# Optimization experiments

Hardware: AMD Instinct MI355X
Metric: run time of the kernel (lower is better)

Reference implementation:

```python
import jax, jax.numpy as jnp
import numpy as np

B, N, W, D, H, E = 8, 10000, 12, 16, 128, 160000
OUT = D  # out_dim must equal in_dim per the reshape in forward


def setup_inputs() -> dict:
    key = jax.random.key(0)
    ks = jax.random.split(key, 13)
    s_ih = 1.0 / np.sqrt(H)
    return {
        "x": jax.random.normal(ks[0], (B, N, W, D), jnp.float32),
        "edge_index": jax.random.randint(ks[1], (2, E), 0, N, dtype=jnp.int64),
        "edge_weight": jax.random.uniform(ks[2], (E,), jnp.float32),
        "W_ih": jax.random.uniform(ks[3], (4 * H, D), jnp.float32, -s_ih, s_ih),
        "W_hh": jax.random.uniform(ks[4], (4 * H, H), jnp.float32, -s_ih, s_ih),
        "b_ih": jax.random.uniform(ks[5], (4 * H,), jnp.float32, -s_ih, s_ih),
        "b_hh": jax.random.uniform(ks[6], (4 * H,), jnp.float32, -s_ih, s_ih),
        "gcn1_w": jax.random.normal(ks[7], (H, H), jnp.float32) * s_ih,
        "gcn1_b": jnp.zeros((H,), jnp.float32),
        "gcn2_w": jax.random.normal(ks[8], (H, H), jnp.float32) * s_ih,
        "gcn2_b": jnp.zeros((H,), jnp.float32),
        "fc_w": jax.random.uniform(ks[9], (OUT, H), jnp.float32, -s_ih, s_ih),
        "fc_b": jax.random.uniform(ks[10], (OUT,), jnp.float32, -s_ih, s_ih),
    }


def reference(x, edge_index, edge_weight, W_ih, W_hh, b_ih, b_hh,
              gcn1_w, gcn1_b, gcn2_w, gcn2_b, fc_w, fc_b):
    Bb, Nn, T, Din = x.shape
    Hh = W_hh.shape[1]
    xs = x.reshape(Bb * Nn, T, Din)

    # --- LSTM over time, keep final hidden state (torch gate order i,f,g,o) ---
    bias = b_ih + b_hh
    def step(carry, xt):
        h, c = carry
        z = xt @ W_ih.T + h @ W_hh.T + bias  # (B*N, 4H)
        i, f, g, o = jnp.split(z, 4, axis=-1)
        c = jax.nn.sigmoid(f) * c + jax.nn.sigmoid(i) * jnp.tanh(g)
        h = jax.nn.sigmoid(o) * jnp.tanh(c)
        return (h, c), None
    h0 = jnp.zeros((Bb * Nn, Hh), x.dtype)
    (h_last, _), _ = jax.lax.scan(step, (h0, h0), jnp.swapaxes(xs, 0, 1))
    h = h_last.reshape(Bb, Nn, Hh)

    # --- GCN normalization with added self-loops (PyG GCNConv semantics) ---
    src, dst = edge_index[0], edge_index[1]
    loop = jnp.arange(Nn)
    src_f = jnp.concatenate([src, loop])
    dst_f = jnp.concatenate([dst, loop])
    w_f = jnp.concatenate([edge_weight, jnp.ones((Nn,), edge_weight.dtype)])
    deg = jnp.zeros((Nn,), w_f.dtype).at[dst_f].add(w_f)
    dinv = jnp.where(deg > 0, jax.lax.rsqrt(jnp.where(deg > 0, deg, 1.0)), 0.0)
    norm = dinv[src_f] * w_f * dinv[dst_f]  # (E+N,)

    def gcn(hx, wgt, b):
        xl = hx @ wgt.T                                  # (B, N, H)
        msg = xl[:, src_f, :] * norm[None, :, None]      # (B, E+N, H)
        agg = jnp.zeros_like(xl).at[:, dst_f, :].add(msg)
        return agg + b

    h = jax.nn.relu(gcn(h, gcn1_w, gcn1_b))
    h = jax.nn.relu(gcn(h, gcn2_w, gcn2_b))
    out = h @ fc_w.T + fc_b                              # (B, N, out_dim)
    return out
```

## Files before the change

### kernel.cpp

```cpp
#include <hip/hip_runtime.h>
#include <math.h>

#define NB 8
#define NN 10000
#define NT 12
#define ND 16
#define NH 128
#define NE 160000
#define BN (NB * NN)

typedef __attribute__((ext_vector_type(8))) short short8v;
typedef __attribute__((ext_vector_type(4))) float f32x4;
typedef unsigned short u16;

#define NL2E  -1.442695041f
#define N2L2E -2.885390082f

__device__ __forceinline__ u16 bf16_rn(float f) {
    unsigned int u = __float_as_uint(f);
    u += 0x7fffu + ((u >> 16) & 1u);
    return (u16)(u >> 16);
}
__device__ __forceinline__ float bf16f(u16 s) {
    return __uint_as_float((unsigned int)s << 16);
}
__device__ __forceinline__ unsigned int pack_split(float f) {
    unsigned int u = __float_as_uint(f);
    unsigned int hh = u >> 16;
    float rem = f - __uint_as_float(u & 0xffff0000u);
    unsigned int hl = bf16_rn(rem);
    return (hl << 16) | hh;
}

__global__ void prep_w_k(const float* __restrict__ Whh, const float* __restrict__ Wih,
                         const float* __restrict__ g1w, const float* __restrict__ g2w,
                         u16* __restrict__ whh_hi, u16* __restrict__ wih_hi2,
                         u16* __restrict__ g1hi, u16* __restrict__ g2hi,
                         float* __restrict__ deg, int* __restrict__ cnt, int* __restrict__ fill)
{
    int i = blockIdx.x * 256 + threadIdx.x;
    if (i < 512 * 128) {
        int j = i >> 7;
        float s = ((j >> 7) == 2) ? N2L2E : NL2E;
        whh_hi[i] = bf16_rn(s * Whh[i]);
    }
    if (i < 512 * 16) {
        int row = i >> 4, d = i & 15;
        float s = ((row >> 7) == 2) ? N2L2E : NL2E;
        u16 h = bf16_rn(s * Wih[i]);
        wih_hi2[row * 32 + d] = h;
        wih_hi2[row * 32 + 16 + d] = h;
    }
    if (i < 128 * 128) {
        g1hi[i] = bf16_rn(g1w[i]);
        g2hi[i] = bf16_rn(g2w[i]);
    }
    if (i < NN) { deg[i] = 1.0f; cnt[i] = 0; fill[i] = 0; }
}

__global__ __launch_bounds__(512, 2) void lstm4d_k(
    const float* __restrict__ x,
    const u16* __restrict__ whh_hi, const u16* __restrict__ wih_hi2,
    const float* __restrict__ bih, const float* __restrict__ bhh,
    u16* __restrict__ hhi_g)
{
    __shared__ __align__(16) u16 Hhi[2][64][128];
    __shared__ __align__(16) u16 Hx[2][64][40];
    const int tid = threadIdx.x;
    const int lane = tid & 63;
    const int wid = tid >> 6;
    const int j0 = wid * 16;
    const int l15 = lane & 15;
    const int lg = lane >> 4;
    const long seq0 = (long)blockIdx.x * 64;
    const int swzr = (l15 & 7) << 3;
    const int xs_seq = tid >> 3;
    const int xd0 = (tid & 7) * 2;

    short8v Bh[4][4];
    short8v b1[4];
    float bv[4];
#pragma unroll
    for (int kt = 0; kt < 4; ++kt)
#pragma unroll
        for (int g = 0; g < 4; ++g) {
            int row = g * NH + j0 + l15;
            Bh[kt][g] = *(const short8v*)(whh_hi + row * NH + kt * 32 + 8 * lg);
        }
#pragma unroll
    for (int g = 0; g < 4; ++g) {
        int row = g * NH + j0 + l15;
        b1[g] = *(const short8v*)(wih_hi2 + row * 32 + 8 * lg);
        bv[g] = (bih[row] + bhh[row]) * ((g == 2) ? N2L2E : NL2E);
    }

    {
        float2 xv = *(const float2*)(x + ((seq0 + xs_seq) * NT + 0) * ND + xd0);
        unsigned int p0 = pack_split(xv.x), p1 = pack_split(xv.y);
        *(ushort2*)&Hx[0][xs_seq][xd0] = make_ushort2((u16)p0, (u16)p1);
        *(ushort2*)&Hx[0][xs_seq][16 + xd0] = make_ushort2((u16)(p0 >> 16), (u16)(p1 >> 16));
    }
    f32x4 c[4];
#pragma unroll
    for (int m = 0; m < 4; ++m) c[m] = (f32x4){0.f, 0.f, 0.f, 0.f};
    __syncthreads();

    for (int t = 0; t < NT; ++t) {
        const int cur = t & 1, nxt = cur ^ 1;
        float2 xv;
        if (t + 1 < NT)
            xv = *(const float2*)(x + ((seq0 + xs_seq) * NT + (t + 1)) * ND + xd0);

#pragma unroll
        for (int m = 0; m < 4; ++m) {
            const int sq = m * 16 + l15;
            short8v xa = *(const short8v*)&Hx[cur][sq][8 * lg];

            f32x4 acc[4];
#pragma unroll
            for (int g = 0; g < 4; ++g)
                acc[g] = (f32x4){bv[g], bv[g], bv[g], bv[g]};

            if (t > 0) {
#pragma unroll
                for (int kt = 0; kt < 4; ++kt) {
                    const int kk = (kt * 32 + 8 * lg) ^ swzr;
                    short8v ah = *(const short8v*)&Hhi[cur][sq][kk];
#pragma unroll
                    for (int g = 0; g < 4; ++g)
                        acc[g] = __builtin_amdgcn_mfma_f32_16x16x32_bf16(ah, Bh[kt][g], acc[g], 0, 0, 0);
                }
            }
#pragma unroll
            for (int g = 0; g < 4; ++g)
                acc[g] = __builtin_amdgcn_mfma_f32_16x16x32_bf16(xa, b1[g], acc[g], 0, 0, 0);

#pragma unroll
            for (int r = 0; r < 4; ++r) {
                const float ui = exp2f(acc[0][r]);
                const float uf = exp2f(acc[1][r]);
                const float ug = exp2f(acc[2][r]);
                const float uo = exp2f(acc[3][r]);
                const float di = 1.f + ui, df = 1.f + uf;
                const float dg = 1.f + ug, dd = 1.f + uo;
                const float r0 = __builtin_amdgcn_rcpf(di * df);
                const float r1 = __builtin_amdgcn_rcpf(dg * dd);
                const float si = r0 * df;
                const float sf = r0 * di;
                const float tg = fmaf(2.f, r1 * dd, -1.f);
                const float so = r1 * dg;
                const float cc = fmaf(sf, c[m][r], si * tg);
                c[m][r] = cc;
                const float uc = exp2f(cc * N2L2E);
                const float rc = __builtin_amdgcn_rcpf(1.f + uc);
                const float hv = fmaf(2.f, so * rc, -so);
                const int sq2 = m * 16 + 4 * lg + r;
                const int jj = (j0 + l15) ^ ((sq2 & 7) << 3);
                Hhi[nxt][sq2][jj] = bf16_rn(hv);
            }
        }

        if (t + 1 < NT) {
            unsigned int p0 = pack_split(xv.x), p1 = pack_split(xv.y);
            *(ushort2*)&Hx[nxt][xs_seq][xd0] = make_ushort2((u16)p0, (u16)p1);
            *(ushort2*)&Hx[nxt][xs_seq][16 + xd0] = make_ushort2((u16)(p0 >> 16), (u16)(p1 >> 16));
        }
        __syncthreads();
    }

    for (int ci = tid; ci < 1024; ci += 512) {
        int s = ci >> 4, g16 = ci & 15;
        int sg = g16 ^ (s & 7);
        unsigned int sglob = (unsigned int)(seq0 + s);
        unsigned int b = sglob / NN;
        unsigned int n = sglob - b * NN;
        uint4 v = *(const uint4*)&Hhi[0][s][sg * 8];
        *(uint4*)(hhi_g + ((long)n * 8 + b) * NH + g16 * 8) = v;
    }
}

__global__ __launch_bounds__(512) void gemmx4_k(
    const u16* __restrict__ Ah, const u16* __restrict__ Whi,
    u16* __restrict__ out)
{
    const int tid = threadIdx.x;
    const int lane = tid & 63;
    const int wid = tid >> 6;
    const int j0 = wid * 16;
    const int l15 = lane & 15;
    const int lg = lane >> 4;
    const long row0 = (long)blockIdx.x * 64;

    short8v Bh[4];
#pragma unroll
    for (int kt = 0; kt < 4; ++kt)
        Bh[kt] = *(const short8v*)(Whi + (j0 + l15) * NH + kt * 32 + 8 * lg);

#pragma unroll
    for (int m = 0; m < 4; ++m) {
        f32x4 acc = (f32x4){0.f, 0.f, 0.f, 0.f};
#pragma unroll
        for (int kt = 0; kt < 4; ++kt) {
            long ar = (row0 + m * 16 + l15) * NH + kt * 32 + 8 * lg;
            short8v ah = *(const short8v*)(Ah + ar);
            acc = __builtin_amdgcn_mfma_f32_16x16x32_bf16(ah, Bh[kt], acc, 0, 0, 0);
        }
#pragma unroll
        for (int r = 0; r < 4; ++r)
            out[(row0 + m * 16 + 4 * lg + r) * NH + j0 + l15] = bf16_rn(acc[r]);
    }
}

__global__ void degacc_k(const int* __restrict__ ei, const float* __restrict__ ew,
                         float* deg, int* cnt) {
    int e = blockIdx.x * 256 + threadIdx.x;
    if (e < NE) {
        int d = ei[NE + e];
        atomicAdd(&deg[d], ew[e]);
        atomicAdd(&cnt[d], 1);
    }
}

__global__ __launch_bounds__(1024) void scan_k(const int* __restrict__ cnt,
                                               int* __restrict__ rowp,
                                               const float* __restrict__ deg,
                                               float* __restrict__ dinv) {
    for (int idx = threadIdx.x; idx < NN; idx += 1024) {
        float d = deg[idx];
        dinv[idx] = d > 0.f ? rsqrtf(d) : 0.f;
    }
    __shared__ int sA[1024];
    __shared__ int sB[1024];
    const int tid = threadIdx.x;
    const int CH = 10;
    int base = tid * CH;
    int local[CH];
    int ssum = 0;
#pragma unroll
    for (int i = 0; i < CH; ++i) {
        int idx = base + i;
        int v = (idx < NN) ? cnt[idx] : 0;
        local[i] = v; ssum += v;
    }
    int* src = sA; int* dst = sB;
    src[tid] = ssum;
    __syncthreads();
    for (int off = 1; off < 1024; off <<= 1) {
        int v = src[tid];
        if (tid >= off) v += src[tid - off];
        dst[tid] = v;
        __syncthreads();
        int* tmp = src; src = dst; dst = tmp;
    }
    int run = src[tid] - ssum;
#pragma unroll
    for (int i = 0; i < CH; ++i) {
        int idx = base + i;
        if (idx < NN) rowp[idx] = run;
        run += local[i];
    }
    if (tid == 1023) rowp[NN] = src[1023];
}

__global__ void scatter_k(const int* __restrict__ ei, const float* __restrict__ ew,
                          const float* __restrict__ dinv, const int* __restrict__ rowp,
                          int* fill, int* __restrict__ col, float* __restrict__ val)
{
    int e = blockIdx.x * 256 + threadIdx.x;
    if (e >= NE) return;
    int srcn = ei[e], d = ei[NE + e];
    int pos = rowp[d] + atomicAdd(&fill[d], 1);
    col[pos] = srcn;
    val[pos] = dinv[srcn] * ew[e] * dinv[d];
}

template<int EMIT>
__global__ __launch_bounds__(256) void gather6_k(const u16* __restrict__ xlb,
    const int* __restrict__ rowp, const int* __restrict__ col,
    const float* __restrict__ val, const float* __restrict__ dinv,
    const float* __restrict__ bias,
    u16* __restrict__ ohi,
    const float* __restrict__ fcw, const float* __restrict__ fcb,
    float* __restrict__ out)
{
    __shared__ float hrow[8][132];
    __shared__ float wl[16][132];
    const int n = blockIdx.x;
    const int tid = threadIdx.x;
    const int q = tid & 31;
    if (EMIT == 1) {
        for (int l = tid; l < 16 * 128; l += 256)
            wl[l >> 7][l & 127] = fcw[l];
    }
    const float dn = dinv[n];
    const float sn = dn * dn;
    float4 acc;
    {
        ushort4 u = *(const ushort4*)(xlb + (long)n * 1024 + tid * 4);
        acc.x = sn * bf16f(u.x); acc.y = sn * bf16f(u.y);
        acc.z = sn * bf16f(u.z); acc.w = sn * bf16f(u.w);
    }
    int e = rowp[n];
    const int e1 = rowp[n + 1];
    for (; e + 2 <= e1; e += 2) {
        const int s0 = col[e], s1 = col[e + 1];
        const float w0 = val[e], w1 = val[e + 1];
        const ushort4 u0 = *(const ushort4*)(xlb + (long)s0 * 1024 + tid * 4);
        const ushort4 u1 = *(const ushort4*)(xlb + (long)s1 * 1024 + tid * 4);
        acc.x = fmaf(w0, bf16f(u0.x), acc.x); acc.y = fmaf(w0, bf16f(u0.y), acc.y);
        acc.z = fmaf(w0, bf16f(u0.z), acc.z); acc.w = fmaf(w0, bf16f(u0.w), acc.w);
        acc.x = fmaf(w1, bf16f(u1.x), acc.x); acc.y = fmaf(w1, bf16f(u1.y), acc.y);
        acc.z = fmaf(w1, bf16f(u1.z), acc.z); acc.w = fmaf(w1, bf16f(u1.w), acc.w);
    }
    if (e < e1) {
        const int s0 = col[e];
        const float w0 = val[e];
        const ushort4 u0 = *(const ushort4*)(xlb + (long)s0 * 1024 + tid * 4);
        acc.x = fmaf(w0, bf16f(u0.x), acc.x); acc.y = fmaf(w0, bf16f(u0.y), acc.y);
        acc.z = fmaf(w0, bf16f(u0.z), acc.z); acc.w = fmaf(w0, bf16f(u0.w), acc.w);
    }
    const float4 bb = ((const float4*)bias)[q];
    const float o0 = fmaxf(acc.x + bb.x, 0.f);
    const float o1 = fmaxf(acc.y + bb.y, 0.f);
    const float o2 = fmaxf(acc.z + bb.z, 0.f);
    const float o3 = fmaxf(acc.w + bb.w, 0.f);
    if (EMIT == 0) {
        ushort4 h4 = make_ushort4(bf16_rn(o0), bf16_rn(o1), bf16_rn(o2), bf16_rn(o3));
        *(ushort4*)(ohi + (long)n * 1024 + tid * 4) = h4;
    } else {
        const int b = tid >> 5;
        *(float4*)&hrow[b][q * 4] = make_float4(o0, o1, o2, o3);
        __syncthreads();
        if (tid < 128) {
            const int b2 = tid >> 4, o = tid & 15;
            float a = fcb[o];
#pragma unroll 8
            for (int k = 0; k < NH; ++k) a = fmaf(hrow[b2][k], wl[o][k], a);
            out[((long)b2 * NN + n) * 16 + o] = a;
        }
    }
}

extern "C" void kernel_launch(void* const* d_in, const int* in_sizes, int n_in,
                              void* d_out, int out_size, void* d_ws, size_t ws_size,
                              hipStream_t stream)
{
    const float* x   = (const float*)d_in[0];
    const int*   ei  = (const int*)d_in[1];
    const float* ew  = (const float*)d_in[2];
    const float* Wih = (const float*)d_in[3];
    const float* Whh = (const float*)d_in[4];
    const float* bih = (const float*)d_in[5];
    const float* bhh = (const float*)d_in[6];
    const float* g1w = (const float*)d_in[7];
    const float* g1b = (const float*)d_in[8];
    const float* g2w = (const float*)d_in[9];
    const float* g2b = (const float*)d_in[10];
    const float* fcw = (const float*)d_in[11];
    const float* fcb = (const float*)d_in[12];
    float* out = (float*)d_out;

    char* ws = (char*)d_ws;
    u16* whh_hi  = (u16*)(ws + 0);
    u16* wih_hi2 = (u16*)(ws + 131072);
    u16* g1hi    = (u16*)(ws + 196608);
    u16* g2hi    = (u16*)(ws + 229376);
    float* deg   = (float*)(ws + 262144);
    float* dinv  = (float*)(ws + 303104);
    int*   cnt   = (int*)(ws + 344064);
    int*   fill  = (int*)(ws + 385024);
    int*   rowp  = (int*)(ws + 425984);
    int*   col   = (int*)(ws + 466176);
    float* val   = (float*)(ws + 1106176);
    u16* hhi     = (u16*)(ws + 2097152);
    u16* xlb     = (u16*)(ws + 22577152);

    prep_w_k<<<256, 256, 0, stream>>>(Whh, Wih, g1w, g2w, whh_hi, wih_hi2,
                                      g1hi, g2hi, deg, cnt, fill);
    lstm4d_k<<<BN / 64, 512, 0, stream>>>(x, whh_hi, wih_hi2, bih, bhh, hhi);

    degacc_k<<<(NE + 255) / 256, 256, 0, stream>>>(ei, ew, deg, cnt);
    scan_k<<<1, 1024, 0, stream>>>(cnt, rowp, deg, dinv);
    scatter_k<<<(NE + 255) / 256, 256, 0, stream>>>(ei, ew, dinv, rowp, fill, col, val);

    gemmx4_k<<<BN / 64, 512, 0, stream>>>(hhi, g1hi, xlb);
    gather6_k<0><<<NN, 256, 0, stream>>>(xlb, rowp, col, val, dinv, g1b,
                                         hhi, nullptr, nullptr, nullptr);
    gemmx4_k<<<BN / 64, 512, 0, stream>>>(hhi, g2hi, xlb);
    gather6_k<1><<<NN, 256, 0, stream>>>(xlb, rowp, col, val, dinv, g2b,
                                         nullptr, fcw, fcb, out);
}
```

Baseline: 477.3 us.

## Fuse GCN weight GEMM into gather kernel by aggregating before transform

```diff
diff --git a/kernel.cpp b/kernel.cpp
--- a/kernel.cpp
+++ b/kernel.cpp
@@ -179,38 +179,6 @@
     }
 }
 
-__global__ __launch_bounds__(512) void gemmx4_k(
-    const u16* __restrict__ Ah, const u16* __restrict__ Whi,
-    u16* __restrict__ out)
-{
-    const int tid = threadIdx.x;
-    const int lane = tid & 63;
-    const int wid = tid >> 6;
-    const int j0 = wid * 16;
-    const int l15 = lane & 15;
-    const int lg = lane >> 4;
-    const long row0 = (long)blockIdx.x * 64;
-
-    short8v Bh[4];
-#pragma unroll
-    for (int kt = 0; kt < 4; ++kt)
-        Bh[kt] = *(const short8v*)(Whi + (j0 + l15) * NH + kt * 32 + 8 * lg);
-
-#pragma unroll
-    for (int m = 0; m < 4; ++m) {
-        f32x4 acc = (f32x4){0.f, 0.f, 0.f, 0.f};
-#pragma unroll
-        for (int kt = 0; kt < 4; ++kt) {
-            long ar = (row0 + m * 16 + l15) * NH + kt * 32 + 8 * lg;
-            short8v ah = *(const short8v*)(Ah + ar);
-            acc = __builtin_amdgcn_mfma_f32_16x16x32_bf16(ah, Bh[kt], acc, 0, 0, 0);
-        }
-#pragma unroll
-        for (int r = 0; r < 4; ++r)
-            out[(row0 + m * 16 + 4 * lg + r) * NH + j0 + l15] = bf16_rn(acc[r]);
-    }
-}
-
 __global__ void degacc_k(const int* __restrict__ ei, const float* __restrict__ ew,
                          float* deg, int* cnt) {
     int e = blockIdx.x * 256 + threadIdx.x;
@@ -274,63 +242,93 @@
     val[pos] = dinv[srcn] * ew[e] * dinv[d];
 }
 
-template<int EMIT>
-__global__ __launch_bounds__(256) void gather6_k(const u16* __restrict__ xlb,
+template<int LAST>
+__global__ __launch_bounds__(256) void gcn_fused_k(const u16* __restrict__ hin,
     const int* __restrict__ rowp, const int* __restrict__ col,
     const float* __restrict__ val, const float* __restrict__ dinv,
-    const float* __restrict__ bias,
-    u16* __restrict__ ohi,
+    const float* __restrict__ bias, const u16* __restrict__ Whi,
+    u16* __restrict__ hout,
     const float* __restrict__ fcw, const float* __restrict__ fcb,
     float* __restrict__ out)
 {
+    __shared__ __align__(16) u16 Ag[16][128];
+    __shared__ __align__(16) u16 Ou[8][128];
     __shared__ float hrow[8][132];
     __shared__ float wl[16][132];
     const int n = blockIdx.x;
     const int tid = threadIdx.x;
+    const int b = tid >> 5;
     const int q = tid & 31;
-    if (EMIT == 1) {
+
+    if (tid < 128) *(uint4*)&Ag[8 + (tid >> 4)][(tid & 15) * 8] = make_uint4(0, 0, 0, 0);
+    if (LAST) {
         for (int l = tid; l < 16 * 128; l += 256)
             wl[l >> 7][l & 127] = fcw[l];
     }
+
     const float dn = dinv[n];
     const float sn = dn * dn;
-    float4 acc;
+    float4 accA, accB = make_float4(0.f, 0.f, 0.f, 0.f);
     {
-        ushort4 u = *(const ushort4*)(xlb + (long)n * 1024 + tid * 4);
-        acc.x = sn * bf16f(u.x); acc.y = sn * bf16f(u.y);
-        acc.z = sn * bf16f(u.z); acc.w = sn * bf16f(u.w);
+        ushort4 u = *(const ushort4*)(hin + (long)n * 1024 + tid * 4);
+        accA.x = sn * bf16f(u.x); accA.y = sn * bf16f(u.y);
+        accA.z = sn * bf16f(u.z); accA.w = sn * bf16f(u.w);
     }
     int e = rowp[n];
     const int e1 = rowp[n + 1];
     for (; e + 2 <= e1; e += 2) {
         const int s0 = col[e], s1 = col[e + 1];
         const float w0 = val[e], w1 = val[e + 1];
-        const ushort4 u0 = *(const ushort4*)(xlb + (long)s0 * 1024 + tid * 4);
-        const ushort4 u1 = *(const ushort4*)(xlb + (long)s1 * 1024 + tid * 4);
-        acc.x = fmaf(w0, bf16f(u0.x), acc.x); acc.y = fmaf(w0, bf16f(u0.y), acc.y);
-        acc.z = fmaf(w0, bf16f(u0.z), acc.z); acc.w = fmaf(w0, bf16f(u0.w), acc.w);
-        acc.x = fmaf(w1, bf16f(u1.x), acc.x); acc.y = fmaf(w1, bf16f(u1.y), acc.y);
-        acc.z = fmaf(w1, bf16f(u1.z), acc.z); acc.w = fmaf(w1, bf16f(u1.w), acc.w);
+        const ushort4 u0 = *(const ushort4*)(hin + (long)s0 * 1024 + tid * 4);
+        const ushort4 u1 = *(const ushort4*)(hin + (long)s1 * 1024 + tid * 4);
+        accA.x = fmaf(w0, bf16f(u0.x), accA.x); accA.y = fmaf(w0, bf16f(u0.y), accA.y);
+        accA.z = fmaf(w0, bf16f(u0.z), accA.z); accA.w = fmaf(w0, bf16f(u0.w), accA.w);
+        accB.x = fmaf(w1, bf16f(u1.x), accB.x); accB.y = fmaf(w1, bf16f(u1.y), accB.y);
+        accB.z = fmaf(w1, bf16f(u1.z), accB.z); accB.w = fmaf(w1, bf16f(u1.w), accB.w);
     }
     if (e < e1) {
         const int s0 = col[e];
         const float w0 = val[e];
-        const ushort4 u0 = *(const ushort4*)(xlb + (long)s0 * 1024 + tid * 4);
-        acc.x = fmaf(w0, bf16f(u0.x), acc.x); acc.y = fmaf(w0, bf16f(u0.y), acc.y);
-        acc.z = fmaf(w0, bf16f(u0.z), acc.z); acc.w = fmaf(w0, bf16f(u0.w), acc.w);
-    }
-    const float4 bb = ((const float4*)bias)[q];
-    const float o0 = fmaxf(acc.x + bb.x, 0.f);
-    const float o1 = fmaxf(acc.y + bb.y, 0.f);
-    const float o2 = fmaxf(acc.z + bb.z, 0.f);
-    const float o3 = fmaxf(acc.w + bb.w, 0.f);
-    if (EMIT == 0) {
-        ushort4 h4 = make_ushort4(bf16_rn(o0), bf16_rn(o1), bf16_rn(o2), bf16_rn(o3));
-        *(ushort4*)(ohi + (long)n * 1024 + tid * 4) = h4;
-    } else {
-        const int b = tid >> 5;
-        *(float4*)&hrow[b][q * 4] = make_float4(o0, o1, o2, o3);
-        __syncthreads();
+        const ushort4 u0 = *(const ushort4*)(hin + (long)s0 * 1024 + tid * 4);
+        accA.x = fmaf(w0, bf16f(u0.x), accA.x); accA.y = fmaf(w0, bf16f(u0.y), accA.y);
+        accA.z = fmaf(w0, bf16f(u0.z), accA.z); accA.w = fmaf(w0, bf16f(u0.w), accA.w);
+    }
+    {
+        ushort4 a4 = make_ushort4(bf16_rn(accA.x + accB.x), bf16_rn(accA.y + accB.y),
+                                  bf16_rn(accA.z + accB.z), bf16_rn(accA.w + accB.w));
+        *(ushort4*)&Ag[b][(q * 4) ^ ((b & 7) << 3)] = a4;
+    }
+    __syncthreads();
+
+    const int lane = tid & 63;
+    const int wid = tid >> 6;
+    const int l15 = lane & 15;
+    const int lg = lane >> 4;
+    const int swzA = (l15 & 7) << 3;
+#pragma unroll
+    for (int jt = 0; jt < 2; ++jt) {
+        const int j0 = (wid * 2 + jt) * 16;
+        f32x4 acc = (f32x4){0.f, 0.f, 0.f, 0.f};
+#pragma unroll
+        for (int kt = 0; kt < 4; ++kt) {
+            short8v ah = *(const short8v*)&Ag[l15][(kt * 32 + 8 * lg) ^ swzA];
+            short8v bh = *(const short8v*)(Whi + (j0 + l15) * NH + kt * 32 + 8 * lg);
+            acc = __builtin_amdgcn_mfma_f32_16x16x32_bf16(ah, bh, acc, 0, 0, 0);
+        }
+        if (lg < 2) {
+            const float bj = bias[j0 + l15];
+#pragma unroll
+            for (int r = 0; r < 4; ++r) {
+                const int row = 4 * lg + r;
+                const float v = fmaxf(acc[r] + bj, 0.f);
+                if (LAST) hrow[row][j0 + l15] = v;
+                else      Ou[row][j0 + l15] = bf16_rn(v);
+            }
+        }
+    }
+    __syncthreads();
+
+    if (LAST) {
         if (tid < 128) {
             const int b2 = tid >> 4, o = tid & 15;
             float a = fcb[o];
@@ -338,6 +336,9 @@
             for (int k = 0; k < NH; ++k) a = fmaf(hrow[b2][k], wl[o][k], a);
             out[((long)b2 * NN + n) * 16 + o] = a;
         }
+    } else {
+        if (tid < 128)
+            *(uint4*)(hout + (long)n * 1024 + tid * 8) = *(const uint4*)&Ou[tid >> 4][(tid & 15) * 8];
     }
 }
 
@@ -373,7 +374,7 @@
     int*   col   = (int*)(ws + 466176);
     float* val   = (float*)(ws + 1106176);
     u16* hhi     = (u16*)(ws + 2097152);
-    u16* xlb     = (u16*)(ws + 22577152);
+    u16* h1      = (u16*)(ws + 22577152);
 
     prep_w_k<<<256, 256, 0, stream>>>(Whh, Wih, g1w, g2w, whh_hi, wih_hi2,
                                       g1hi, g2hi, deg, cnt, fill);
@@ -383,10 +384,8 @@
     scan_k<<<1, 1024, 0, stream>>>(cnt, rowp, deg, dinv);
     scatter_k<<<(NE + 255) / 256, 256, 0, stream>>>(ei, ew, dinv, rowp, fill, col, val);
 
-    gemmx4_k<<<BN / 64, 512, 0, stream>>>(hhi, g1hi, xlb);
-    gather6_k<0><<<NN, 256, 0, stream>>>(xlb, rowp, col, val, dinv, g1b,
-                                         hhi, nullptr, nullptr, nullptr);
-    gemmx4_k<<<BN / 64, 512, 0, stream>>>(hhi, g2hi, xlb);
-    gather6_k<1><<<NN, 256, 0, stream>>>(xlb, rowp, col, val, dinv, g2b,
-                                         nullptr, fcw, fcb, out);
-}
+    gcn_fused_k<0><<<NN, 256, 0, stream>>>(hhi, rowp, col, val, dinv, g1b, g1hi,
+                                           h1, nullptr, nullptr, nullptr);
+    gcn_fused_k<1><<<NN, 256, 0, stream>>>(h1, rowp, col, val, dinv, g2b, g2hi,
+                                           nullptr, fcw, fcb, out);
+}
```

Measured after the change: 471.8 us. About the same (-1.2%).
